# Kernel tuning notes

Measured on AMD Instinct MI355X. Metric: run time of the kernel, lower is better.

## Reference

```python
import jax, jax.numpy as jnp
import numpy as np

N_NODES = 100000
N_EDGES = 800000
N_GRAPHS = 4000
EMB = 128      # node_emb_dims
HID = 256      # hidden_dims
FP = 2048      # fingerprint_dims
FIELD_DIMS = {"atom_type": 120, "degree": 12, "charge": 10}


def setup_inputs() -> dict:
    key = jax.random.key(0)
    ks = iter(jax.random.split(key, 40))
    p = lambda shape: jax.random.normal(next(ks), shape, dtype=jnp.float32) * 0.02
    inp = {
        "atom_idx": jax.random.randint(next(ks), (N_NODES,), 0, FIELD_DIMS["atom_type"]),
        "degree_idx": jax.random.randint(next(ks), (N_NODES,), 0, FIELD_DIMS["degree"]),
        "charge_idx": jax.random.randint(next(ks), (N_NODES,), 0, FIELD_DIMS["charge"]),
        "edge_index": jax.random.randint(next(ks), (2, N_EDGES), 0, N_NODES),
        "batch": jnp.sort(jax.random.randint(next(ks), (N_NODES,), 0, N_GRAPHS)),
        "fingerprint": jax.random.normal(next(ks), (N_GRAPHS, FP), dtype=jnp.float32),
        # FFM projector params
        "emb_atom": p((FIELD_DIMS["atom_type"], EMB)),
        "emb_degree": p((FIELD_DIMS["degree"], EMB)),
        "emb_charge": p((FIELD_DIMS["charge"], EMB)),
        "proj_w1": p((3 * EMB, EMB)), "proj_b1": jnp.zeros((EMB,), jnp.float32),
        "proj_w2": p((EMB, EMB)), "proj_b2": jnp.zeros((EMB,), jnp.float32),
        # fingerprint linear
        "fp_w": p((FP, HID)), "fp_b": jnp.zeros((HID,), jnp.float32),
        # GCN layers
        "conv_w0": p((EMB, HID)), "conv_b0": jnp.zeros((HID,), jnp.float32),
        "conv_w1": p((HID, HID)), "conv_b1": jnp.zeros((HID,), jnp.float32),
        "conv_w2": p((HID, HID)), "conv_b2": jnp.zeros((HID,), jnp.float32),
        "conv_w3": p((HID, HID)), "conv_b3": jnp.zeros((HID,), jnp.float32),
        # head
        "lin1_w": p((2 * HID, HID // 2)), "lin1_b": jnp.zeros((HID // 2,), jnp.float32),
        "lin2_w": p((HID // 2, 1)), "lin2_b": jnp.zeros((1,), jnp.float32),
    }
    return inp


def gcn_conv(x, w, b, src, dst, n):
    # PyG GCNConv: linear, add self-loops, symmetric norm, scatter-add at dst, + bias
    xw = x @ w
    loop = jnp.arange(n)
    src_f = jnp.concatenate([src, loop])
    dst_f = jnp.concatenate([dst, loop])
    deg = jax.ops.segment_sum(jnp.ones_like(dst_f, dtype=x.dtype), dst_f, num_segments=n)
    dinv = jax.lax.rsqrt(deg)  # deg >= 1 thanks to self-loops
    norm = dinv[src_f] * dinv[dst_f]                       # [E+N]
    msg = xw[src_f] * norm[:, None]                        # [E+N, HID]
    return jax.ops.segment_sum(msg, dst_f, num_segments=n) + b


def reference(atom_idx, degree_idx, charge_idx, edge_index, batch, fingerprint,
              emb_atom, emb_degree, emb_charge,
              proj_w1, proj_b1, proj_w2, proj_b2, fp_w, fp_b,
              conv_w0, conv_b0, conv_w1, conv_b1, conv_w2, conv_b2, conv_w3, conv_b3,
              lin1_w, lin1_b, lin2_w, lin2_b):
    # FieldAwareFactorizationMachine projector (vectorized over all nodes)
    e = jnp.concatenate([emb_atom[atom_idx], emb_degree[degree_idx], emb_charge[charge_idx]], axis=-1)
    h = jax.nn.relu(e @ proj_w1 + proj_b1) @ proj_w2 + proj_b2   # [N, EMB]
    src, dst = edge_index[0], edge_index[1]
    for w, b in ((conv_w0, conv_b0), (conv_w1, conv_b1), (conv_w2, conv_b2), (conv_w3, conv_b3)):
        h = jax.nn.relu(gcn_conv(h, w, b, src, dst, N_NODES))
    pooled = jax.ops.segment_sum(h, batch, num_segments=N_GRAPHS)  # scatter sum pooling
    fp_emb = fingerprint @ fp_w + fp_b
    z = jnp.concatenate([fp_emb, pooled], axis=-1)                 # [B, 2*HID]
    z = jax.nn.relu(z @ lin1_w + lin1_b)
    return z @ lin2_w + lin2_b                                     # [B, 1]
```

## Files before the change

kernel.cpp:

```cpp
#include <hip/hip_runtime.h>
#include <stdint.h>

#define NN 100000
#define NE 800000
#define NG 4000
#define NBLK ((NN + 255) / 256)

typedef __attribute__((ext_vector_type(8))) short s16x8;
typedef __attribute__((ext_vector_type(4))) float f32x4;
typedef __attribute__((ext_vector_type(2))) float f32x2;

__device__ __forceinline__ float b2f(unsigned short u) {
    return __uint_as_float(((unsigned int)u) << 16);
}
__device__ __forceinline__ unsigned short f2b(float f) {
    unsigned int x = __float_as_uint(f);
    x = x + 0x7FFFu + ((x >> 16) & 1u);
    return (unsigned short)(x >> 16);
}
__device__ __forceinline__ s16x8 cvt8(const float* __restrict__ p) {
    float4 a = *(const float4*)p;
    float4 b = *(const float4*)(p + 4);
    s16x8 r = {(short)f2b(a.x), (short)f2b(a.y), (short)f2b(a.z), (short)f2b(a.w),
               (short)f2b(b.x), (short)f2b(b.y), (short)f2b(b.z), (short)f2b(b.w)};
    return r;
}

__device__ __forceinline__ void gload16(const void* g, void* l) {
    __builtin_amdgcn_global_load_lds((const __attribute__((address_space(1))) unsigned int*)g,
                                     (__attribute__((address_space(3))) unsigned int*)l, 16, 0, 0);
}

__device__ __forceinline__ void acc8(f32x2* acc, s16x8 r) {
    const unsigned int* u = (const unsigned int*)&r;
#pragma unroll
    for (int q = 0; q < 4; ++q) {
        unsigned int w = u[q];
        f32x2 x;
        x[0] = __uint_as_float(w << 16);
        x[1] = __uint_as_float(w & 0xFFFF0000u);
        asm("v_pk_add_f32 %0, %1, %0" : "+v"(acc[q]) : "v"(x));
    }
}

__global__ void k_count(const int* __restrict__ dst, int* __restrict__ cnt) {
    int e = blockIdx.x * 256 + threadIdx.x;
    if (e < NE) atomicAdd(&cnt[dst[e]], 1);
}

__global__ void k_dinv(const int* __restrict__ cnt, float* __restrict__ dinv) {
    int n = blockIdx.x * 256 + threadIdx.x;
    if (n < NN) dinv[n] = rsqrtf((float)(cnt[n] + 1));
}

__global__ __launch_bounds__(256) void k_bsum(const int* __restrict__ cnt, int* __restrict__ bsum) {
    __shared__ int s[256];
    int i = blockIdx.x * 256 + threadIdx.x;
    s[threadIdx.x] = (i < NN) ? cnt[i] : 0;
    __syncthreads();
    for (int off = 128; off; off >>= 1) {
        if (threadIdx.x < off) s[threadIdx.x] += s[threadIdx.x + off];
        __syncthreads();
    }
    if (threadIdx.x == 0) bsum[blockIdx.x] = s[0];
}

__global__ __launch_bounds__(512) void k_bscan(const int* __restrict__ bsum, int* __restrict__ bpre) {
    __shared__ int s[512];
    int t = threadIdx.x;
    int v = (t < NBLK) ? bsum[t] : 0;
    s[t] = v;
    __syncthreads();
    for (int off = 1; off < 512; off <<= 1) {
        int u = (t >= off) ? s[t - off] : 0;
        __syncthreads();
        s[t] += u;
        __syncthreads();
    }
    if (t < NBLK) bpre[t] = s[t] - v;
}

__global__ __launch_bounds__(256) void k_rowptr(const int* __restrict__ cnt, const int* __restrict__ bpre,
                                                int* __restrict__ row_ptr, int* __restrict__ cursor) {
    __shared__ int s[256];
    int t = threadIdx.x;
    int i = blockIdx.x * 256 + t;
    int v = (i < NN) ? cnt[i] : 0;
    s[t] = v;
    __syncthreads();
    for (int off = 1; off < 256; off <<= 1) {
        int u = (t >= off) ? s[t - off] : 0;
        __syncthreads();
        s[t] += u;
        __syncthreads();
    }
    if (i < NN) {
        int excl = bpre[blockIdx.x] + s[t] - v;
        row_ptr[i] = excl;
        cursor[i] = excl;
        if (i == NN - 1) row_ptr[NN] = NE;
    }
}

__global__ void k_fill(const int* __restrict__ src, const int* __restrict__ dst,
                       int* __restrict__ cursor, int* __restrict__ colA) {
    int e = blockIdx.x * 256 + threadIdx.x;
    if (e < NE) {
        int d = dst[e];
        int p = atomicAdd(&cursor[d], 1);
        colA[p] = src[e];
    }
}

__global__ void k_t(const float* __restrict__ src, unsigned short* __restrict__ dst, int KN, int ln) {
    int i = blockIdx.x * 256 + threadIdx.x;
    if (i < KN) {
        int k = i >> ln, n = i & ((1 << ln) - 1);
        dst[(size_t)n * (KN >> ln) + k] = f2b(src[i]);
    }
}

__global__ void k_cvt(const float* __restrict__ src, unsigned short* __restrict__ dst, int n8) {
    int i = blockIdx.x * 256 + threadIdx.x;
    if (i < n8) *(s16x8*)&dst[(size_t)i * 8] = cvt8(&src[(size_t)i * 8]);
}

__global__ void k_binit(float* __restrict__ fe, const float* __restrict__ b) {
    int i = blockIdx.x * 256 + threadIdx.x;
    fe[i] = b[i & 255];
}

__global__ void k_z(const float* __restrict__ fe, unsigned short* __restrict__ zcat) {
    int i = blockIdx.x * 256 + threadIdx.x;
    int g = i >> 8, c = i & 255;
    zcat[(size_t)g * 512 + c] = f2b(fe[i]);
}

template <bool GATHER, bool BIAS, bool RELU, bool CBF16>
__global__ __launch_bounds__(256) void k_mm(
    const unsigned short* __restrict__ A, const unsigned short* __restrict__ Bt,
    void* __restrict__ Cv, const float* __restrict__ bias, int M, int N, int K,
    const int* __restrict__ ai, const int* __restrict__ di, const int* __restrict__ ci,
    const float* __restrict__ ea, const float* __restrict__ ed, const float* __restrict__ ec) {
    __shared__ unsigned short As[128 * 40];
    __shared__ unsigned short Bs[128 * 40];
    const int tid = threadIdx.x;
    const int row0 = blockIdx.x * 128, col0 = blockIdx.y * 128;
    const int lane = tid & 63, wid = tid >> 6;
    const int wrow = (wid >> 1) * 64, wcol = (wid & 1) * 64;
    const int lr = lane & 15, lk8 = (lane >> 4) * 8;

    const int sr = tid >> 1;
    const int skc = (tid & 1) * 16;
    const int agrow = row0 + sr;
    const int bgrow = col0 + sr;
    int ia = 0, idg = 0, ic = 0;
    if (GATHER && agrow < M) { ia = ai[agrow] * 128; idg = di[agrow] * 128; ic = ci[agrow] * 128; }

    f32x4 acc[4][4] = {};

    for (int kb = 0; kb < K; kb += 32) {
        if (kb) __syncthreads();
#pragma unroll
        for (int c = 0; c < 2; ++c) {
            int kloc = skc + c * 8;
            s16x8 v = {};
            if (agrow < M) {
                if (GATHER) {
                    int kg = kb + kloc;
                    const float* p = (kg < 128) ? (ea + ia + kg)
                                   : (kg < 256) ? (ed + idg + kg - 128)
                                                : (ec + ic + kg - 256);
                    v = cvt8(p);
                } else {
                    v = *(const s16x8*)&A[(size_t)agrow * K + kb + kloc];
                }
            }
            *(s16x8*)&As[sr * 40 + kloc] = v;
            s16x8 w = *(const s16x8*)&Bt[(size_t)bgrow * K + kb + kloc];
            *(s16x8*)&Bs[sr * 40 + kloc] = w;
        }
        __syncthreads();
        s16x8 af[4], bfr[4];
#pragma unroll
        for (int f = 0; f < 4; ++f)
            af[f] = *(const s16x8*)&As[(wrow + f * 16 + lr) * 40 + lk8];
#pragma unroll
        for (int f = 0; f < 4; ++f)
            bfr[f] = *(const s16x8*)&Bs[(wcol + f * 16 + lr) * 40 + lk8];
#pragma unroll
        for (int fm = 0; fm < 4; ++fm)
#pragma unroll
            for (int fn = 0; fn < 4; ++fn)
                acc[fm][fn] = __builtin_amdgcn_mfma_f32_16x16x32_bf16(af[fm], bfr[fn], acc[fm][fn], 0, 0, 0);
    }
#pragma unroll
    for (int fm = 0; fm < 4; ++fm) {
#pragma unroll
        for (int r = 0; r < 4; ++r) {
            int row = row0 + wrow + fm * 16 + (lane >> 4) * 4 + r;
            if (row < M) {
#pragma unroll
                for (int fn = 0; fn < 4; ++fn) {
                    int col = col0 + wcol + fn * 16 + lr;
                    float v = acc[fm][fn][r];
                    if (BIAS) v += bias[col];
                    if (RELU) v = fmaxf(v, 0.f);
                    if (CBF16) ((unsigned short*)Cv)[(size_t)row * N + col] = f2b(v);
                    else       ((float*)Cv)[(size_t)row * N + col] = v;
                }
            }
        }
    }
}

template <bool BIAS, bool RELU, bool CBF16, bool SPLITK, bool PRES>
__global__ __launch_bounds__(256) void k_mmA(
    const unsigned short* __restrict__ A, const unsigned short* __restrict__ Bt,
    void* __restrict__ Cv, const float* __restrict__ bias, const float* __restrict__ pres,
    int M, int N, int K, int kc) {
    __shared__ unsigned short As[2][128 * 32];
    __shared__ unsigned short Bs[2][128 * 32];
    const int tid = threadIdx.x;
    const int row0 = blockIdx.x * 128, col0 = blockIdx.y * 128;
    const int lane = tid & 63, wid = tid >> 6;
    const int wrow = (wid >> 1) * 64, wcol = (wid & 1) * 64;
    const int lr = lane & 15, lk8 = (lane >> 4) * 8;

    const int k0 = SPLITK ? blockIdx.z * kc : 0;
    const int nt = (SPLITK ? kc : K) / 32;

    const int sra = wid * 32 + (lane >> 2);
    const int sca = (lane & 3) * 8;
    const unsigned short* a0 = A + (size_t)min(row0 + sra, M - 1) * K + sca + k0;
    const unsigned short* a1 = A + (size_t)min(row0 + sra + 16, M - 1) * K + sca + k0;
    const unsigned short* b0 = Bt + (size_t)(col0 + sra) * K + sca + k0;
    const unsigned short* b1 = Bt + (size_t)(col0 + sra + 16) * K + sca + k0;
    const int lo0 = (wid * 2 + 0) * 512;
    const int lo1 = (wid * 2 + 1) * 512;

    f32x4 acc[4][4] = {};

    gload16(a0, &As[0][lo0]);
    gload16(a1, &As[0][lo1]);
    gload16(b0, &Bs[0][lo0]);
    gload16(b1, &Bs[0][lo1]);
    __syncthreads();

    int cur = 0;
    for (int t = 0; t < nt; ++t) {
        if (t + 1 < nt) {
            int kb = (t + 1) * 32;
            gload16(a0 + kb, &As[cur ^ 1][lo0]);
            gload16(a1 + kb, &As[cur ^ 1][lo1]);
            gload16(b0 + kb, &Bs[cur ^ 1][lo0]);
            gload16(b1 + kb, &Bs[cur ^ 1][lo1]);
        }
        s16x8 af[4], bfr[4];
#pragma unroll
        for (int f = 0; f < 4; ++f)
            af[f] = *(const s16x8*)&As[cur][(wrow + f * 16 + lr) * 32 + lk8];
#pragma unroll
        for (int f = 0; f < 4; ++f)
            bfr[f] = *(const s16x8*)&Bs[cur][(wcol + f * 16 + lr) * 32 + lk8];
#pragma unroll
        for (int fm = 0; fm < 4; ++fm)
#pragma unroll
            for (int fn = 0; fn < 4; ++fn)
                acc[fm][fn] = __builtin_amdgcn_mfma_f32_16x16x32_bf16(af[fm], bfr[fn], acc[fm][fn], 0, 0, 0);
        __syncthreads();
        cur ^= 1;
    }
#pragma unroll
    for (int fm = 0; fm < 4; ++fm) {
#pragma unroll
        for (int r = 0; r < 4; ++r) {
            int row = row0 + wrow + fm * 16 + (lane >> 4) * 4 + r;
            if (row < M) {
                float pr = PRES ? pres[row] : 1.f;
#pragma unroll
                for (int fn = 0; fn < 4; ++fn) {
                    int col = col0 + wcol + fn * 16 + lr;
                    float v = acc[fm][fn][r];
                    if (SPLITK) {
                        atomicAdd(&((float*)Cv)[(size_t)row * N + col], v);
                    } else {
                        if (BIAS) v += bias[col];
                        if (RELU) v = fmaxf(v, 0.f);
                        if (PRES) v *= pr;
                        if (CBF16) ((unsigned short*)Cv)[(size_t)row * N + col] = f2b(v);
                        else       ((float*)Cv)[(size_t)row * N + col] = v;
                    }
                }
            }
        }
    }
}

template <int WPN, bool FUSE>
__global__ __launch_bounds__(256) void k_scat3(const unsigned short* __restrict__ xw,
                                               unsigned short* __restrict__ hout,
                                               const float* __restrict__ dinv,
                                               const int* __restrict__ row_ptr,
                                               const int* __restrict__ colA,
                                               const float* __restrict__ bias) {
    constexpr int W = WPN * 128;
    constexpr int NPW = 4 / WPN;
    const int wid = threadIdx.x >> 6, lane = threadIdx.x & 63;
    const int grp = lane >> 4, li = lane & 15;
    const int v = (blockIdx.x * 4 + wid) * NPW + grp / WPN;
    const int cs = (WPN == 2) ? (grp & 1) * 128 : 0;
    const int c0 = cs + li * 8;

    f32x2 acc[4] = {};
    const int beg = row_ptr[v], end = row_ptr[v + 1];
    int p = beg;
    for (; p + 1 < end; p += 2) {
        int s0 = colA[p], s1 = colA[p + 1];
        s16x8 r0 = *(const s16x8*)&xw[(size_t)s0 * W + c0];
        s16x8 r1 = *(const s16x8*)&xw[(size_t)s1 * W + c0];
        acc8(acc, r0);
        acc8(acc, r1);
    }
    if (p < end) {
        s16x8 r0 = *(const s16x8*)&xw[(size_t)colA[p] * W + c0];
        acc8(acc, r0);
    }

    const float dv = dinv[v];
    s16x8 rs = *(const s16x8*)&xw[(size_t)v * W + c0];
    unsigned short o[8];
#pragma unroll
    for (int j = 0; j < 8; ++j) {
        float a = acc[j >> 1][j & 1];
        a += b2f((unsigned short)rs[j]);
        a *= dv;
        if (FUSE) a = fmaxf(a + bias[c0 + j], 0.f);
        o[j] = f2b(a);
    }
    *(s16x8*)&hout[(size_t)v * W + c0] = *(const s16x8*)o;
}

__global__ void k_bounds(const int* __restrict__ batch, int* __restrict__ gstart) {
    int n = blockIdx.x * 256 + threadIdx.x;
    if (n >= NN) return;
    int b = batch[n];
    if (n == 0) {
        for (int g = 0; g <= b; ++g) gstart[g] = 0;
    } else {
        int pb = batch[n - 1];
        if (pb != b)
            for (int g = pb + 1; g <= b; ++g) gstart[g] = n;
    }
    if (n == NN - 1) {
        for (int g = b + 1; g <= NG; ++g) gstart[g] = NN;
    }
}

__global__ __launch_bounds__(64) void k_pool(const unsigned short* __restrict__ h,
                                             const int* __restrict__ gstart,
                                             unsigned short* __restrict__ zcat) {
    int g = blockIdx.x;
    int lane = threadIdx.x;
    int c0 = lane * 4;
    int beg = gstart[g], end = gstart[g + 1];
    float a0 = 0.f, a1 = 0.f, a2 = 0.f, a3 = 0.f;
    for (int n = beg; n < end; ++n) {
        ushort4 r = *(const ushort4*)&h[(size_t)n * 256 + c0];
        a0 += b2f(r.x); a1 += b2f(r.y); a2 += b2f(r.z); a3 += b2f(r.w);
    }
    ushort4 o;
    o.x = f2b(a0); o.y = f2b(a1); o.z = f2b(a2); o.w = f2b(a3);
    *(ushort4*)&zcat[(size_t)g * 512 + 256 + c0] = o;
}

__global__ __launch_bounds__(256) void k_dot(const float* __restrict__ z1,
                                             const float* __restrict__ w2,
                                             const float* __restrict__ b2,
                                             float* __restrict__ out) {
    int wid = threadIdx.x >> 6, lane = threadIdx.x & 63;
    int g = blockIdx.x * 4 + wid;
    float s = z1[(size_t)g * 128 + lane] * w2[lane]
            + z1[(size_t)g * 128 + 64 + lane] * w2[64 + lane];
#pragma unroll
    for (int off = 32; off; off >>= 1) s += __shfl_xor(s, off);
    if (lane == 0) out[g] = s + b2[0];
}

extern "C" void kernel_launch(void* const* d_in, const int* in_sizes, int n_in,
                              void* d_out, int out_size, void* d_ws, size_t ws_size,
                              hipStream_t stream) {
    const int* atom_idx   = (const int*)d_in[0];
    const int* degree_idx = (const int*)d_in[1];
    const int* charge_idx = (const int*)d_in[2];
    const int* edge_index = (const int*)d_in[3];
    const int* batch      = (const int*)d_in[4];
    const float* fingerprint = (const float*)d_in[5];
    const float* emb_atom   = (const float*)d_in[6];
    const float* emb_degree = (const float*)d_in[7];
    const float* emb_charge = (const float*)d_in[8];
    const float* proj_w1 = (const float*)d_in[9];
    const float* proj_b1 = (const float*)d_in[10];
    const float* proj_w2 = (const float*)d_in[11];
    const float* proj_b2 = (const float*)d_in[12];
    const float* fp_w = (const float*)d_in[13];
    const float* fp_b = (const float*)d_in[14];
    const float* conv_w[4] = {(const float*)d_in[15], (const float*)d_in[17],
                              (const float*)d_in[19], (const float*)d_in[21]};
    const float* conv_b[4] = {(const float*)d_in[16], (const float*)d_in[18],
                              (const float*)d_in[20], (const float*)d_in[22]};
    const float* lin1_w = (const float*)d_in[23];
    const float* lin1_b = (const float*)d_in[24];
    const float* lin2_w = (const float*)d_in[25];
    const float* lin2_b = (const float*)d_in[26];
    float* out = (float*)d_out;

    const int* src = edge_index;
    const int* dst = edge_index + NE;

    char* p = (char*)d_ws;
    auto carve = [&](size_t bytes) { void* r = (void*)p; p += (bytes + 255) & ~(size_t)255; return r; };
    unsigned short* bufA = (unsigned short*)carve((size_t)NN * 256 * 2);
    unsigned short* bufB = (unsigned short*)carve((size_t)NN * 256 * 2);
    int*   cnt     = (int*)carve((size_t)NN * 4);
    float* dinv    = (float*)carve((size_t)NN * 4);
    int*   row_ptr = (int*)carve((size_t)(NN + 1) * 4);
    int*   cursor  = (int*)carve((size_t)(NN + 1) * 4);
    int*   colA    = (int*)carve((size_t)NE * 4);
    int*   gstart  = (int*)carve((size_t)(NG + 1) * 4);
    float* fp_emb  = (float*)carve((size_t)NG * 256 * 4);
    int*   bsum    = (int*)carve((size_t)NBLK * 4);
    int*   bpre    = (int*)carve((size_t)NBLK * 4);
    unsigned short* w1t  = (unsigned short*)carve((size_t)128 * 384 * 2);
    unsigned short* w2t  = (unsigned short*)carve((size_t)128 * 128 * 2);
    unsigned short* cwt[4];
    cwt[0] = (unsigned short*)carve((size_t)256 * 128 * 2);
    for (int l = 1; l < 4; ++l) cwt[l] = (unsigned short*)carve((size_t)256 * 256 * 2);
    unsigned short* fpwt = (unsigned short*)carve((size_t)256 * 2048 * 2);
    unsigned short* fpbf = (unsigned short*)carve((size_t)NG * 2048 * 2);
    unsigned short* l1wt = (unsigned short*)carve((size_t)128 * 512 * 2);
    unsigned short* zcat = (unsigned short*)carve((size_t)NG * 512 * 2);
    float* z1      = (float*)carve((size_t)NG * 128 * 4);

    hipMemsetAsync(cnt, 0, (size_t)NN * 4, stream);
    k_count<<<(NE + 255) / 256, 256, 0, stream>>>(dst, cnt);
    k_dinv<<<(NN + 255) / 256, 256, 0, stream>>>(cnt, dinv);
    k_bsum<<<NBLK, 256, 0, stream>>>(cnt, bsum);
    k_bscan<<<1, 512, 0, stream>>>(bsum, bpre);
    k_rowptr<<<NBLK, 256, 0, stream>>>(cnt, bpre, row_ptr, cursor);
    k_fill<<<(NE + 255) / 256, 256, 0, stream>>>(src, dst, cursor, colA);

    k_t<<<(49152 + 255) / 256, 256, 0, stream>>>(proj_w1, w1t, 49152, 7);
    k_t<<<(16384 + 255) / 256, 256, 0, stream>>>(proj_w2, w2t, 16384, 7);
    k_t<<<(32768 + 255) / 256, 256, 0, stream>>>(conv_w[0], cwt[0], 32768, 8);
    for (int l = 1; l < 4; ++l)
        k_t<<<(65536 + 255) / 256, 256, 0, stream>>>(conv_w[l], cwt[l], 65536, 8);
    k_t<<<(524288 + 255) / 256, 256, 0, stream>>>(fp_w, fpwt, 524288, 8);
    k_t<<<(65536 + 255) / 256, 256, 0, stream>>>(lin1_w, l1wt, 65536, 7);
    k_cvt<<<(NG * 2048 / 8 + 255) / 256, 256, 0, stream>>>(fingerprint, fpbf, NG * 2048 / 8);

    k_binit<<<NG, 256, 0, stream>>>(fp_emb, fp_b);
    k_mmA<false, false, false, true, false><<<dim3((NG + 127) / 128, 2, 4), 256, 0, stream>>>(
        fpbf, fpwt, fp_emb, nullptr, nullptr, NG, 256, 2048, 512);
    k_z<<<NG, 256, 0, stream>>>(fp_emb, zcat);

    const int mg = (NN + 127) / 128;

    k_mm<true, true, true, true><<<dim3(mg, 1), 256, 0, stream>>>(
        nullptr, w1t, bufA, proj_b1, NN, 128, 384,
        atom_idx, degree_idx, charge_idx, emb_atom, emb_degree, emb_charge);
    k_mmA<true, false, true, false, true><<<dim3(mg, 1), 256, 0, stream>>>(
        bufA, w2t, bufB, proj_b2, dinv, NN, 128, 128, 0);

    k_scat3<1, false><<<NN / 16, 256, 0, stream>>>(bufB, bufA, dinv, row_ptr, colA, nullptr);
    k_mmA<true, true, true, false, false><<<dim3(mg, 2), 256, 0, stream>>>(
        bufA, cwt[0], bufB, conv_b[0], nullptr, NN, 256, 128, 0);

    for (int l = 1; l < 4; ++l) {
        k_mmA<false, false, true, false, true><<<dim3(mg, 2), 256, 0, stream>>>(
            bufB, cwt[l], bufA, nullptr, dinv, NN, 256, 256, 0);
        k_scat3<2, true><<<NN / 8, 256, 0, stream>>>(bufA, bufB, dinv, row_ptr, colA, conv_b[l]);
    }

    k_bounds<<<(NN + 255) / 256, 256, 0, stream>>>(batch, gstart);
    k_pool<<<NG, 64, 0, stream>>>(bufB, gstart, zcat);

    k_mmA<true, true, false, false, false><<<dim3((NG + 127) / 128, 1), 256, 0, stream>>>(
        zcat, l1wt, z1, lin1_b, nullptr, NG, 128, 512, 0);
    k_dot<<<NG / 4, 256, 0, stream>>>(z1, lin2_w, lin2_b, out);
}
```

Baseline: 749.1 us.

## Add full-width 512-thread GEMM, batch weight transposes, fuse dinv, unroll gather

Adds a new GEMM kernel where one 512-thread block computes all 256 output columns of a 128-row tile, so each A tile is loaded once instead of twice across two column blocks. It also folds the dinv computation into the row-pointer scan, merges six weight transpose launches into one multi-segment launch, and unrolls the neighbour gather in the scatter kernel from two to four loads per iteration. The aim is less A-tile traffic and fewer launches. The cost is larger shared memory and more threads per block, which may lower occupancy.

```diff
diff --git a/kernel.cpp b/kernel.cpp
--- a/kernel.cpp
+++ b/kernel.cpp
@@ -46,11 +46,6 @@
 __global__ void k_count(const int* __restrict__ dst, int* __restrict__ cnt) {
     int e = blockIdx.x * 256 + threadIdx.x;
     if (e < NE) atomicAdd(&cnt[dst[e]], 1);
-}
-
-__global__ void k_dinv(const int* __restrict__ cnt, float* __restrict__ dinv) {
-    int n = blockIdx.x * 256 + threadIdx.x;
-    if (n < NN) dinv[n] = rsqrtf((float)(cnt[n] + 1));
 }
 
 __global__ __launch_bounds__(256) void k_bsum(const int* __restrict__ cnt, int* __restrict__ bsum) {
@@ -81,7 +76,8 @@
 }
 
 __global__ __launch_bounds__(256) void k_rowptr(const int* __restrict__ cnt, const int* __restrict__ bpre,
-                                                int* __restrict__ row_ptr, int* __restrict__ cursor) {
+                                                int* __restrict__ row_ptr, int* __restrict__ cursor,
+                                                float* __restrict__ dinv) {
     __shared__ int s[256];
     int t = threadIdx.x;
     int i = blockIdx.x * 256 + t;
@@ -98,6 +94,7 @@
         int excl = bpre[blockIdx.x] + s[t] - v;
         row_ptr[i] = excl;
         cursor[i] = excl;
+        dinv[i] = rsqrtf((float)(v + 1));
         if (i == NN - 1) row_ptr[NN] = NE;
     }
 }
@@ -112,12 +109,22 @@
     }
 }
 
-__global__ void k_t(const float* __restrict__ src, unsigned short* __restrict__ dst, int KN, int ln) {
+struct TArgs {
+    const float* src[7];
+    unsigned short* dst[7];
+    int kn[7];
+    int ln[7];
+    int off[8];
+};
+
+__global__ __launch_bounds__(256) void k_prep(TArgs a) {
     int i = blockIdx.x * 256 + threadIdx.x;
-    if (i < KN) {
-        int k = i >> ln, n = i & ((1 << ln) - 1);
-        dst[(size_t)n * (KN >> ln) + k] = f2b(src[i]);
-    }
+    if (i >= a.off[7]) return;
+    int s = 0;
+    while (i >= a.off[s + 1]) ++s;
+    int j = i - a.off[s];
+    int k = j >> a.ln[s], n = j & ((1 << a.ln[s]) - 1);
+    a.dst[s][(size_t)n * (a.kn[s] >> a.ln[s]) + k] = f2b(a.src[s][j]);
 }
 
 __global__ void k_cvt(const float* __restrict__ src, unsigned short* __restrict__ dst, int n8) {
@@ -297,6 +304,83 @@
     }
 }
 
+template <bool BIAS, bool RELU, bool CBF16, bool PRES>
+__global__ __launch_bounds__(512) void k_mmB(
+    const unsigned short* __restrict__ A, const unsigned short* __restrict__ Bt,
+    void* __restrict__ Cv, const float* __restrict__ bias, const float* __restrict__ pres,
+    int M, int K) {
+    constexpr int N = 256;
+    __shared__ unsigned short As[2][128 * 32];
+    __shared__ unsigned short Bs[2][256 * 32];
+    const int tid = threadIdx.x;
+    const int row0 = blockIdx.x * 128;
+    const int lane = tid & 63, wid = tid >> 6;
+    const int wrow = (wid >> 2) * 64, wcol = (wid & 3) * 64;
+    const int lr = lane & 15, lk8 = (lane >> 4) * 8;
+
+    const int nt = K / 32;
+
+    const int rsub = lane >> 2;
+    const int csub = (lane & 3) * 8;
+    const unsigned short* ga  = A  + (size_t)min(row0 + wid * 16 + rsub, M - 1) * K + csub;
+    const unsigned short* gb0 = Bt + (size_t)(wid * 16 + rsub) * K + csub;
+    const unsigned short* gb1 = Bt + (size_t)(128 + wid * 16 + rsub) * K + csub;
+    const int la  = wid * 512;
+    const int lb0 = wid * 512;
+    const int lb1 = (8 + wid) * 512;
+
+    f32x4 acc[4][4] = {};
+
+    gload16(ga, &As[0][la]);
+    gload16(gb0, &Bs[0][lb0]);
+    gload16(gb1, &Bs[0][lb1]);
+    __syncthreads();
+
+    int cur = 0;
+    for (int t = 0; t < nt; ++t) {
+        if (t + 1 < nt) {
+            int kb = (t + 1) * 32;
+            gload16(ga + kb, &As[cur ^ 1][la]);
+            gload16(gb0 + kb, &Bs[cur ^ 1][lb0]);
+            gload16(gb1 + kb, &Bs[cur ^ 1][lb1]);
+        }
+        s16x8 af[4], bfr[4];
+#pragma unroll
+        for (int f = 0; f < 4; ++f)
+            af[f] = *(const s16x8*)&As[cur][(wrow + f * 16 + lr) * 32 + lk8];
+#pragma unroll
+        for (int f = 0; f < 4; ++f)
+            bfr[f] = *(const s16x8*)&Bs[cur][(wcol + f * 16 + lr) * 32 + lk8];
+#pragma unroll
+        for (int fm = 0; fm < 4; ++fm)
+#pragma unroll
+            for (int fn = 0; fn < 4; ++fn)
+                acc[fm][fn] = __builtin_amdgcn_mfma_f32_16x16x32_bf16(af[fm], bfr[fn], acc[fm][fn], 0, 0, 0);
+        __syncthreads();
+        cur ^= 1;
+    }
+#pragma unroll
+    for (int fm = 0; fm < 4; ++fm) {
+#pragma unroll
+        for (int r = 0; r < 4; ++r) {
+            int row = row0 + wrow + fm * 16 + (lane >> 4) * 4 + r;
+            if (row < M) {
+                float pr = PRES ? pres[row] : 1.f;
+#pragma unroll
+                for (int fn = 0; fn < 4; ++fn) {
+                    int col = wcol + fn * 16 + lr;
+                    float v = acc[fm][fn][r];
+                    if (BIAS) v += bias[col];
+                    if (RELU) v = fmaxf(v, 0.f);
+                    if (PRES) v *= pr;
+                    if (CBF16) ((unsigned short*)Cv)[(size_t)row * N + col] = f2b(v);
+                    else       ((float*)Cv)[(size_t)row * N + col] = v;
+                }
+            }
+        }
+    }
+}
+
 template <int WPN, bool FUSE>
 __global__ __launch_bounds__(256) void k_scat3(const unsigned short* __restrict__ xw,
                                                unsigned short* __restrict__ hout,
@@ -312,23 +396,28 @@
     const int cs = (WPN == 2) ? (grp & 1) * 128 : 0;
     const int c0 = cs + li * 8;
 
+    const float dv = dinv[v];
+    s16x8 rs = *(const s16x8*)&xw[(size_t)v * W + c0];
+
     f32x2 acc[4] = {};
     const int beg = row_ptr[v], end = row_ptr[v + 1];
     int p = beg;
-    for (; p + 1 < end; p += 2) {
-        int s0 = colA[p], s1 = colA[p + 1];
+    for (; p + 3 < end; p += 4) {
+        int s0 = colA[p], s1 = colA[p + 1], s2 = colA[p + 2], s3 = colA[p + 3];
         s16x8 r0 = *(const s16x8*)&xw[(size_t)s0 * W + c0];
         s16x8 r1 = *(const s16x8*)&xw[(size_t)s1 * W + c0];
+        s16x8 r2 = *(const s16x8*)&xw[(size_t)s2 * W + c0];
+        s16x8 r3 = *(const s16x8*)&xw[(size_t)s3 * W + c0];
         acc8(acc, r0);
         acc8(acc, r1);
-    }
-    if (p < end) {
+        acc8(acc, r2);
+        acc8(acc, r3);
+    }
+    for (; p < end; ++p) {
         s16x8 r0 = *(const s16x8*)&xw[(size_t)colA[p] * W + c0];
         acc8(acc, r0);
     }
 
-    const float dv = dinv[v];
-    s16x8 rs = *(const s16x8*)&xw[(size_t)v * W + c0];
     unsigned short o[8];
 #pragma unroll
     for (int j = 0; j < 8; ++j) {
@@ -444,19 +533,29 @@
 
     hipMemsetAsync(cnt, 0, (size_t)NN * 4, stream);
     k_count<<<(NE + 255) / 256, 256, 0, stream>>>(dst, cnt);
-    k_dinv<<<(NN + 255) / 256, 256, 0, stream>>>(cnt, dinv);
     k_bsum<<<NBLK, 256, 0, stream>>>(cnt, bsum);
     k_bscan<<<1, 512, 0, stream>>>(bsum, bpre);
-    k_rowptr<<<NBLK, 256, 0, stream>>>(cnt, bpre, row_ptr, cursor);
+    k_rowptr<<<NBLK, 256, 0, stream>>>(cnt, bpre, row_ptr, cursor, dinv);
     k_fill<<<(NE + 255) / 256, 256, 0, stream>>>(src, dst, cursor, colA);
 
-    k_t<<<(49152 + 255) / 256, 256, 0, stream>>>(proj_w1, w1t, 49152, 7);
-    k_t<<<(16384 + 255) / 256, 256, 0, stream>>>(proj_w2, w2t, 16384, 7);
-    k_t<<<(32768 + 255) / 256, 256, 0, stream>>>(conv_w[0], cwt[0], 32768, 8);
-    for (int l = 1; l < 4; ++l)
-        k_t<<<(65536 + 255) / 256, 256, 0, stream>>>(conv_w[l], cwt[l], 65536, 8);
-    k_t<<<(524288 + 255) / 256, 256, 0, stream>>>(fp_w, fpwt, 524288, 8);
-    k_t<<<(65536 + 255) / 256, 256, 0, stream>>>(lin1_w, l1wt, 65536, 7);
+    {
+        TArgs a;
+        const float* s7[7] = {proj_w1, proj_w2, conv_w[0], conv_w[1], conv_w[2], conv_w[3], fp_w};
+        unsigned short* d7[7] = {w1t, w2t, cwt[0], cwt[1], cwt[2], cwt[3], fpwt};
+        int kn7[7] = {49152, 16384, 32768, 65536, 65536, 65536, 524288};
+        int ln7[7] = {7, 7, 8, 8, 8, 8, 8};
+        int o = 0;
+        for (int s = 0; s < 7; ++s) { a.src[s] = s7[s]; a.dst[s] = d7[s]; a.kn[s] = kn7[s]; a.ln[s] = ln7[s]; a.off[s] = o; o += kn7[s]; }
+        a.off[7] = o;
+        k_prep<<<(o + 255) / 256, 256, 0, stream>>>(a);
+    }
+    {
+        TArgs a;
+        a.src[0] = lin1_w; a.dst[0] = l1wt; a.kn[0] = 65536; a.ln[0] = 7; a.off[0] = 0;
+        for (int s = 1; s < 7; ++s) { a.src[s] = lin1_w; a.dst[s] = l1wt; a.kn[s] = 0; a.ln[s] = 0; a.off[s] = 65536; }
+        a.off[7] = 65536;
+        k_prep<<<(65536 + 255) / 256, 256, 0, stream>>>(a);
+    }
     k_cvt<<<(NG * 2048 / 8 + 255) / 256, 256, 0, stream>>>(fingerprint, fpbf, NG * 2048 / 8);
 
     k_binit<<<NG, 256, 0, stream>>>(fp_emb, fp_b);
@@ -473,12 +572,12 @@
         bufA, w2t, bufB, proj_b2, dinv, NN, 128, 128, 0);
 
     k_scat3<1, false><<<NN / 16, 256, 0, stream>>>(bufB, bufA, dinv, row_ptr, colA, nullptr);
-    k_mmA<true, true, true, false, false><<<dim3(mg, 2), 256, 0, stream>>>(
-        bufA, cwt[0], bufB, conv_b[0], nullptr, NN, 256, 128, 0);
+    k_mmB<true, true, true, false><<<mg, 512, 0, stream>>>(
+        bufA, cwt[0], bufB, conv_b[0], nullptr, NN, 128);
 
     for (int l = 1; l < 4; ++l) {
-        k_mmA<false, false, true, false, true><<<dim3(mg, 2), 256, 0, stream>>>(
-            bufB, cwt[l], bufA, nullptr, dinv, NN, 256, 256, 0);
+        k_mmB<false, false, true, true><<<mg, 512, 0, stream>>>(
+            bufB, cwt[l], bufA, nullptr, dinv, NN, 256);
         k_scat3<2, true><<<NN / 8, 256, 0, stream>>>(bufA, bufB, dinv, row_ptr, colA, conv_b[l]);
     }
 
```

Measured after the change: 709.5 us. -5.3%, faster.
